# Kernel tuning notes

Measured on AMD Instinct MI355X. Metric: run time of the kernel, lower is better.

## Reference

```python
import jax, jax.numpy as jnp
import numpy as np
from jax import lax

C, H, W = 256, 56, 56
KP, STRIDE = 9, 2
M_CH, D, T = 64, 128, 16
TOPK = 32
SIGMA, ALPHA, TAU, EPS = 3.0, 10.0, 10.0, 1e-6
B = 4
N = H * W
PAD = KP // 2


def _build_M_P(h, w, s):
    ys = np.arange(0, h, s)
    xs = np.arange(0, w, s)
    ny, nx = len(ys), len(xs)
    N_, K_ = h * w, ny * nx
    by, bx = np.meshgrid(np.arange(h, dtype=np.float32), np.arange(w, dtype=np.float32), indexing='ij')
    bx = bx.reshape(-1)
    by = by.reshape(-1)
    fx, fy = bx / float(s), by / float(s)
    x0 = np.floor(fx).astype(np.int64)
    y0 = np.floor(fy).astype(np.int64)
    x0c = np.clip(x0, 0, nx - 1)
    x1c = np.clip(x0 + 1, 0, nx - 1)
    y0c = np.clip(y0, 0, ny - 1)
    y1c = np.clip(y0 + 1, 0, ny - 1)
    wx = fx - x0
    wy = fy - y0
    Mm = np.zeros((N_, K_), dtype=np.float32)
    rows = np.arange(N_)
    Mm[rows, y0c * nx + x0c] += (1 - wx) * (1 - wy)
    Mm[rows, y0c * nx + x1c] += wx * (1 - wy)
    Mm[rows, y1c * nx + x0c] += (1 - wx) * wy
    Mm[rows, y1c * nx + x1c] += wx * wy
    rs = Mm.sum(1, keepdims=True)
    rs[rs == 0] = 1.0
    Mm = Mm / rs
    P = np.stack([bx, by], axis=-1).astype(np.float32)  # (N,2) (x,y)
    return Mm, P


def _forward(feature_map, A_bank, pw_w, pw_b, proj_w, proj_b, r, M, P):
    def make_grid(A):  # affine_grid, align_corners=False
        xs = (2.0 * jnp.arange(W, dtype=jnp.float32) + 1.0) / W - 1.0
        ys = (2.0 * jnp.arange(H, dtype=jnp.float32) + 1.0) / H - 1.0
        gy, gx = jnp.meshgrid(ys, xs, indexing='ij')
        base = jnp.stack([gx, gy, jnp.ones_like(gx)], axis=-1)  # (H,W,3)
        return base @ A.T  # (H,W,2) normalized (x,y)

    def grid_sample(grid):  # bilinear, border padding, align_corners=False
        ix = ((grid[..., 0] + 1.0) * W - 1.0) / 2.0
        iy = ((grid[..., 1] + 1.0) * H - 1.0) / 2.0
        x0 = jnp.floor(ix)
        y0 = jnp.floor(iy)
        wx = ix - x0
        wy = iy - y0
        x0c = jnp.clip(x0, 0, W - 1).astype(jnp.int32)
        x1c = jnp.clip(x0 + 1, 0, W - 1).astype(jnp.int32)
        y0c = jnp.clip(y0, 0, H - 1).astype(jnp.int32)
        y1c = jnp.clip(y0 + 1, 0, H - 1).astype(jnp.int32)
        fm = feature_map.reshape(B, C, H * W)
        def g(yc, xc):
            return fm[:, :, (yc * W + xc).reshape(-1)].reshape(B, C, H, W)
        return (g(y0c, x0c) * (1 - wx) * (1 - wy) + g(y0c, x1c) * wx * (1 - wy)
                + g(y1c, x0c) * (1 - wx) * wy + g(y1c, x1c) * wx * wy)

    grids = jax.vmap(make_grid)(A_bank)          # (T,H,W,2)
    warped = jax.vmap(grid_sample)(grids)        # (T,B,C,H,W)

    # unfold(k,pad,stride) -> 1x1 conv -> spatial mean  ==  zero-padded avg-pool then linear
    pm = lax.reduce_window(warped, 0.0, lax.add,
                           (1, 1, 1, KP, KP), (1, 1, 1, STRIDE, STRIDE),
                           [(0, 0), (0, 0), (0, 0), (PAD, PAD), (PAD, PAD)]) / (KP * KP)
    Tn, Bn, Cn, Kh, Kw = pm.shape
    K = Kh * Kw
    pm = pm.reshape(Tn, Bn, Cn, K).transpose(0, 1, 3, 2)  # (T,B,K,C)
    x = pm @ pw_w.T + pw_b                                 # (T,B,K,m)
    z = x @ proj_w.T + proj_b                              # (T,B,K,d)
    z = z / jnp.maximum(jnp.linalg.norm(z, axis=-1, keepdims=True), EPS)
    Z = z.transpose(1, 0, 2, 3)                            # (B,T,K,d)

    s = jnp.einsum('btkd,d->btk', Z, r)
    wgt = jax.nn.softmax(TAU * s, axis=1)[..., None]
    g_emb = jnp.sum(wgt * Z, axis=1)                       # (B,K,d)

    E = jnp.einsum('nk,bkd->bnd', M, g_emb)
    E = E / jnp.maximum(jnp.linalg.norm(E, axis=-1, keepdims=True), EPS)

    d2 = jnp.sum((P[:, None, :] - P[None, :, :]) ** 2, axis=-1)  # (N,N)
    G = 1.0 - jnp.exp(-d2 / (2.0 * SIGMA ** 2))
    Saff = jnp.einsum('bnd,bmd->bnm', E, E) * G

    vals, idx = lax.top_k(Saff, TOPK)
    bidx = jnp.arange(B)[:, None, None]
    nidx = jnp.arange(N)[None, :, None]
    S_sp = jnp.zeros_like(Saff).at[bidx, nidx, idx].set(vals)
    A0 = jax.nn.softmax(ALPHA * S_sp, axis=-1) * jax.nn.softmax(ALPHA * S_sp, axis=-2)
    return E, A0


def setup_inputs() -> dict:
    key = jax.random.key(0)
    ks = jax.random.split(key, 6)
    feature_map = jax.random.normal(ks[0], (B, C, H, W), jnp.float32)
    ident = jnp.broadcast_to(jnp.array([[1.0, 0.0, 0.0], [0.0, 1.0, 0.0]], jnp.float32), (T, 2, 3))
    A_bank = ident + 0.1 * jax.random.normal(ks[1], (T, 2, 3), jnp.float32)
    pw_w = jax.random.normal(ks[2], (M_CH, C), jnp.float32) / np.sqrt(C).astype(np.float32)
    pw_b = jnp.zeros((M_CH,), jnp.float32)
    proj_w = jax.random.normal(ks[3], (D, M_CH), jnp.float32) / np.sqrt(M_CH).astype(np.float32)
    proj_b = jnp.zeros((D,), jnp.float32)
    r = 0.01 * jax.random.normal(ks[4], (D,), jnp.float32)
    Mnp, Pnp = _build_M_P(H, W, STRIDE)
    return {'feature_map': feature_map, 'A_bank': A_bank, 'pw_w': pw_w, 'pw_b': pw_b,
            'proj_w': proj_w, 'proj_b': proj_b, 'r': r,
            'M': jnp.asarray(Mnp), 'P': jnp.asarray(Pnp)}


def reference(feature_map, A_bank, pw_w, pw_b, proj_w, proj_b, r, M, P):
    return _forward(feature_map, A_bank, pw_w, pw_b, proj_w, proj_b, r, M, P)
```

## Files before the change

kernel.cpp:

```cpp
#include <hip/hip_runtime.h>
#include <hip/hip_bf16.h>
#include <hip/hip_fp16.h>

#define Hh 56
#define Ww 56
#define Cc 256
#define Tt 16
#define Bb 4
#define Nn 3136
#define Kk 784
#define KX 28
#define Dd 128
#define Mc 64
#define NTOP 32

__global__ __launch_bounds__(128) void k_wc(
    const float* __restrict__ pw_w, const float* __restrict__ pw_b,
    const float* __restrict__ proj_w, const float* __restrict__ proj_b,
    float* __restrict__ wct, float* __restrict__ bc) {
  int c = blockIdx.x;
  int d = threadIdx.x;
  float acc = 0.f;
  for (int m = 0; m < Mc; ++m) acc += proj_w[d * Mc + m] * pw_w[m * Cc + c];
  wct[c * Dd + d] = acc;
  if (c == 0) {
    float bb = proj_b[d];
    for (int m = 0; m < Mc; ++m) bb += proj_w[d * Mc + m] * pw_b[m];
    bc[d] = bb;
  }
}

__global__ __launch_bounds__(256) void k_mix(
    const float* __restrict__ fm, const float* __restrict__ wct, float* __restrict__ y) {
  int blk = blockIdx.x;
  int b = blk / 112;
  int n0 = (blk % 112) * 28;
  int tid = threadIdx.x;
  int d = tid & 127;
  int ng = tid >> 7;
  __shared__ float fm_s[64 * 28];
  __shared__ float wc_s[64 * Dd];
  float acc[14];
#pragma unroll
  for (int j = 0; j < 14; ++j) acc[j] = 0.f;
  const float* fb = fm + (size_t)b * Cc * Nn;
  for (int c0 = 0; c0 < Cc; c0 += 64) {
    for (int i = tid; i < 64 * 28; i += 256) {
      int c = i / 28, kx = i - c * 28;
      fm_s[i] = fb[(size_t)(c0 + c) * Nn + n0 + kx];
    }
    for (int i = tid; i < 64 * Dd; i += 256) wc_s[i] = wct[c0 * Dd + i];
    __syncthreads();
    for (int c = 0; c < 64; ++c) {
      float w = wc_s[c * Dd + d];
#pragma unroll
      for (int j = 0; j < 14; ++j) acc[j] += fm_s[c * 28 + ng * 14 + j] * w;
    }
    __syncthreads();
  }
  float* yo = y + ((size_t)b * Dd + d) * Nn + n0 + ng * 14;
#pragma unroll
  for (int j = 0; j < 14; ++j) yo[j] = acc[j];
}

__global__ __launch_bounds__(256) void k_fused_pool(
    const float* __restrict__ y, const float* __restrict__ Abank,
    const float* __restrict__ bc, float* __restrict__ zt) {
  int idx = blockIdx.x;
  int b = idx & 3;
  int dg = (idx >> 2) & 31;
  int t = idx >> 7;
  __shared__ float wsm[3136];
  __shared__ float rowp[1568];
  int tid = threadIdx.x;
  const float* A = Abank + t * 6;
  float a00 = A[0], a01 = A[1], a02 = A[2], a10 = A[3], a11 = A[4], a12 = A[5];
  int off[13];
  float wxa[13], wya[13];
#pragma unroll
  for (int j = 0; j < 13; ++j) {
    int e = tid + 256 * j;
    if (e < 3136) {
      int h = e / 56, w = e - h * 56;
      float gx = (2.0f * w + 1.0f) / 56.0f - 1.0f;
      float gy = (2.0f * h + 1.0f) / 56.0f - 1.0f;
      float u = a00 * gx + a01 * gy + a02;
      float v = a10 * gx + a11 * gy + a12;
      float ix = ((u + 1.0f) * 56.0f - 1.0f) * 0.5f;
      float iy = ((v + 1.0f) * 56.0f - 1.0f) * 0.5f;
      float x0f = floorf(ix), y0f = floorf(iy);
      wxa[j] = ix - x0f;
      wya[j] = iy - y0f;
      int x0 = (int)x0f, y0 = (int)y0f;
      int x0c = min(max(x0, 0), 55), x1c = min(max(x0 + 1, 0), 55);
      int y0c = min(max(y0, 0), 55), y1c = min(max(y0 + 1, 0), 55);
      off[j] = (y0c * 56 + x0c) | ((x1c - x0c) << 12) | ((y1c - y0c) << 13);
    }
  }
  for (int dd = 0; dd < 4; ++dd) {
    int d = dg * 4 + dd;
    const float* fc = y + ((size_t)b * Dd + d) * Nn;
    float bias = bc[d];
#pragma unroll
    for (int j = 0; j < 13; ++j) {
      int e = tid + 256 * j;
      if (e < 3136) {
        int pk = off[j];
        int base = pk & 4095;
        int dx = (pk >> 12) & 1;
        int dyy = (pk & (1 << 13)) ? 56 : 0;
        float v00 = fc[base], v01 = fc[base + dx];
        float v10 = fc[base + dyy], v11 = fc[base + dyy + dx];
        float wx = wxa[j], wy = wya[j];
        float top = v00 + wx * (v01 - v00);
        float bot = v10 + wx * (v11 - v10);
        wsm[e] = top + wy * (bot - top);
      }
    }
    __syncthreads();
    for (int e = tid; e < 1568; e += 256) {
      int h = e / 28, kx = e - h * 28;
      int xs = 2 * kx - 4;
      int lo = max(xs, 0), hi = min(xs + 8, 55);
      float s = 0.f;
      const float* wr = wsm + h * 56;
      for (int x = lo; x <= hi; ++x) s += wr[x];
      rowp[e] = s;
    }
    __syncthreads();
    float* zo = zt + ((size_t)(t * Bb + b) * Dd + d) * Kk;
    for (int e = tid; e < 784; e += 256) {
      int ky = e / 28, kx = e - ky * 28;
      int ys = 2 * ky - 4;
      int lo = max(ys, 0), hi = min(ys + 8, 55);
      float s = 0.f;
      for (int h = lo; h <= hi; ++h) s += rowp[h * 28 + kx];
      zo[e] = s * (1.0f / 81.0f) + bias;
    }
    __syncthreads();
  }
}

__global__ __launch_bounds__(256) void k_znorm(
    const float* __restrict__ zt, const float* __restrict__ r,
    float* __restrict__ z, float* __restrict__ s_arr) {
  int tb = blockIdx.x / 14;
  int k0 = (blockIdx.x % 14) * 56;
  int tid = threadIdx.x;
  __shared__ float ls[56 * 129];
  const float* zb = zt + (size_t)tb * Dd * Kk + k0;
  for (int i = tid; i < Dd * 56; i += 256) {
    int d = i / 56, kk = i - d * 56;
    ls[kk * 129 + d] = zb[(size_t)d * Kk + kk];
  }
  int lane = tid & 63;
  int wv = tid >> 6;
  float r0 = r[lane], r1 = r[lane + 64];
  __syncthreads();
  for (int p = 0; p < 14; ++p) {
    int k = p * 4 + wv;
    float z0 = ls[k * 129 + lane];
    float z1 = ls[k * 129 + 64 + lane];
    float ss = z0 * z0 + z1 * z1;
    for (int off = 32; off; off >>= 1) ss += __shfl_xor(ss, off);
    float inv = 1.0f / fmaxf(sqrtf(ss), 1e-6f);
    z0 *= inv; z1 *= inv;
    float* zr = z + ((size_t)tb * Kk + k0 + k) * Dd;
    zr[lane] = z0;
    zr[lane + 64] = z1;
    float sd = z0 * r0 + z1 * r1;
    for (int off = 32; off; off >>= 1) sd += __shfl_xor(sd, off);
    if (lane == 0) s_arr[(size_t)tb * Kk + k0 + k] = sd;
  }
}

__global__ __launch_bounds__(128) void k_gemb(
    const float* __restrict__ z, const float* __restrict__ s_arr, float* __restrict__ g) {
  int blk = blockIdx.x;
  int b = blk / Kk, k = blk % Kk;
  int d = threadIdx.x;
  float sv[Tt];
  float mx = -3.4e38f;
#pragma unroll
  for (int t = 0; t < Tt; ++t) {
    sv[t] = s_arr[(t * Bb + b) * Kk + k];
    mx = fmaxf(mx, sv[t]);
  }
  float sum = 0.f;
#pragma unroll
  for (int t = 0; t < Tt; ++t) {
    sv[t] = expf(10.0f * (sv[t] - mx));
    sum += sv[t];
  }
  float isum = 1.0f / sum;
  float acc = 0.f;
#pragma unroll
  for (int t = 0; t < Tt; ++t)
    acc += sv[t] * isum * z[((size_t)(t * Bb + b) * Kk + k) * Dd + d];
  g[((size_t)b * Kk + k) * Dd + d] = acc;
}

__global__ __launch_bounds__(64) void k_E(
    const float* __restrict__ Mmat, const float* __restrict__ g, float* __restrict__ E) {
  int row = blockIdx.x;
  int b = row / Nn, n = row % Nn;
  int y = n / Ww, x = n % Ww;
  int x0 = x >> 1, y0 = y >> 1;
  int x1 = min(x0 + 1, 27), y1 = min(y0 + 1, 27);
  bool hx = (x1 != x0), hy = (y1 != y0);
  int k00 = y0 * 28 + x0, k01 = y0 * 28 + x1, k10 = y1 * 28 + x0, k11 = y1 * 28 + x1;
  const float* Mr = Mmat + (size_t)n * Kk;
  float m00 = Mr[k00];
  float m01 = hx ? Mr[k01] : 0.f;
  float m10 = hy ? Mr[k10] : 0.f;
  float m11 = (hx && hy) ? Mr[k11] : 0.f;
  const float* gb = g + (size_t)b * Kk * Dd;
  int lane = threadIdx.x;
  int l2 = lane + 64;
  float a0 = m00 * gb[k00 * Dd + lane] + m01 * gb[k01 * Dd + lane] +
             m10 * gb[k10 * Dd + lane] + m11 * gb[k11 * Dd + lane];
  float a1 = m00 * gb[k00 * Dd + l2] + m01 * gb[k01 * Dd + l2] +
             m10 * gb[k10 * Dd + l2] + m11 * gb[k11 * Dd + l2];
  float ss = a0 * a0 + a1 * a1;
  for (int off = 32; off; off >>= 1) ss += __shfl_xor(ss, off);
  float inv = 1.0f / fmaxf(sqrtf(ss), 1e-6f);
  E[(size_t)row * Dd + lane] = a0 * inv;
  E[(size_t)row * Dd + l2] = a1 * inv;
}

__global__ __launch_bounds__(256) void k_saff(
    const float* __restrict__ E, const float* __restrict__ P, __half* __restrict__ S) {
  int blk = blockIdx.x;
  int b = blk / 1225;
  int rem = blk % 1225;
  int ti0 = (int)((sqrtf(8.f * rem + 1.f) - 1.f) * 0.5f);
  while ((ti0 + 1) * (ti0 + 2) / 2 <= rem) ++ti0;
  while (ti0 * (ti0 + 1) / 2 > rem) --ti0;
  int tj0 = rem - ti0 * (ti0 + 1) / 2;
  int i0 = ti0 * 64, j0 = tj0 * 64;
  __shared__ __align__(16) float Ei_s[64 * 68];
  __shared__ __align__(16) float Ej_s[64 * 68];
  __shared__ float s_pxi[64], s_pyi[64], s_pxj[64], s_pyj[64];
  int tid = threadIdx.x;
  const float* Eb = E + (size_t)b * Nn * Dd;
  if (tid < 64) {
    s_pxi[tid] = P[(i0 + tid) * 2];
    s_pyi[tid] = P[(i0 + tid) * 2 + 1];
    s_pxj[tid] = P[(j0 + tid) * 2];
    s_pyj[tid] = P[(j0 + tid) * 2 + 1];
  }
  int ti = tid >> 4, tj = tid & 15;
  int ib = ti * 4, jb = tj * 4;
  float acc[4][4];
#pragma unroll
  for (int a = 0; a < 4; ++a)
#pragma unroll
    for (int c = 0; c < 4; ++c) acc[a][c] = 0.f;
  for (int kc = 0; kc < Dd; kc += 64) {
    __syncthreads();
    for (int idx = tid; idx < 64 * 64; idx += 256) {
      int ii = idx >> 6, dd = idx & 63;
      Ei_s[dd * 68 + ii] = Eb[(size_t)(i0 + ii) * Dd + kc + dd];
      Ej_s[dd * 68 + ii] = Eb[(size_t)(j0 + ii) * Dd + kc + dd];
    }
    __syncthreads();
#pragma unroll 8
    for (int kk = 0; kk < 64; ++kk) {
      const float4 a = *reinterpret_cast<const float4*>(&Ei_s[kk * 68 + ib]);
      const float4 q = *reinterpret_cast<const float4*>(&Ej_s[kk * 68 + jb]);
      acc[0][0] += a.x * q.x; acc[0][1] += a.x * q.y; acc[0][2] += a.x * q.z; acc[0][3] += a.x * q.w;
      acc[1][0] += a.y * q.x; acc[1][1] += a.y * q.y; acc[1][2] += a.y * q.z; acc[1][3] += a.y * q.w;
      acc[2][0] += a.z * q.x; acc[2][1] += a.z * q.y; acc[2][2] += a.z * q.z; acc[2][3] += a.z * q.w;
      acc[3][0] += a.w * q.x; acc[3][1] += a.w * q.y; acc[3][2] += a.w * q.z; acc[3][3] += a.w * q.w;
    }
  }
  float outv[4][4];
#pragma unroll
  for (int di = 0; di < 4; ++di) {
    float px = s_pxi[ib + di], py = s_pyi[ib + di];
#pragma unroll
    for (int dj = 0; dj < 4; ++dj) {
      float dx = px - s_pxj[jb + dj];
      float dy = py - s_pyj[jb + dj];
      float gg = 1.0f - __expf(-(dx * dx + dy * dy) * (1.0f / 18.0f));
      outv[di][dj] = acc[di][dj] * gg;
    }
  }
  size_t ob = (size_t)b * Nn * Nn;
#pragma unroll
  for (int di = 0; di < 4; ++di) {
    __half2 h01 = __floats2half2_rn(outv[di][0], outv[di][1]);
    __half2 h23 = __floats2half2_rn(outv[di][2], outv[di][3]);
    __half2* p = reinterpret_cast<__half2*>(&S[ob + (size_t)(i0 + ib + di) * Nn + j0 + jb]);
    p[0] = h01; p[1] = h23;
  }
  if (i0 != j0) {
#pragma unroll
    for (int dj = 0; dj < 4; ++dj) {
      __half2 h01 = __floats2half2_rn(outv[0][dj], outv[1][dj]);
      __half2 h23 = __floats2half2_rn(outv[2][dj], outv[3][dj]);
      __half2* p = reinterpret_cast<__half2*>(&S[ob + (size_t)(j0 + jb + dj) * Nn + i0 + ib]);
      p[0] = h01; p[1] = h23;
    }
  }
}

__global__ __launch_bounds__(256) void k_topk(
    const __half* __restrict__ S16, const float* __restrict__ E,
    const float* __restrict__ P, float* __restrict__ topv, int* __restrict__ topi,
    float* __restrict__ dr, float* __restrict__ dc) {
  int row = blockIdx.x;
  int b = row / Nn, irow = row % Nn;
  int tid = threadIdx.x;
  const unsigned* Sr = reinterpret_cast<const unsigned*>(S16 + (size_t)row * Nn);
  __shared__ unsigned hist[256 * 8];
  __shared__ unsigned scan_s[256];
  __shared__ unsigned bcast[2];
  __shared__ unsigned sel_eq, sel_slot;
  __shared__ int sel_idx[NTOP];
  __shared__ float drow_s;
  unsigned pk[7];
#pragma unroll
  for (int j = 0; j < 7; ++j) {
    int c2 = tid + 256 * j;
    unsigned u = (c2 < Nn / 2) ? Sr[c2] : 0u;
    unsigned h0 = u & 0xFFFFu, h1 = u >> 16;
    unsigned k0 = h0 ^ ((h0 & 0x8000u) ? 0xFFFFu : 0x8000u);
    unsigned k1 = h1 ^ ((h1 & 0x8000u) ? 0xFFFFu : 0x8000u);
    if (c2 >= Nn / 2) { k0 = 0u; k1 = 0u; }
    pk[j] = k0 | (k1 << 16);
  }
  if (tid == 0) { sel_eq = 0; sel_slot = 0; drow_s = 0.f; }
  unsigned prefix = 0;
  unsigned k = NTOP;
  for (int pass = 0; pass < 2; ++pass) {
    int shift = 8 - 8 * pass;
    unsigned pmask = pass ? 0xFF00u : 0u;
#pragma unroll
    for (int i = 0; i < 8; ++i) hist[tid * 8 + i] = 0;
    __syncthreads();
#pragma unroll
    for (int j = 0; j < 7; ++j) {
      unsigned k0 = pk[j] & 0xFFFFu, k1 = pk[j] >> 16;
      if ((k0 & pmask) == (prefix & pmask))
        atomicAdd(&hist[((k0 >> shift) & 255u) * 8 + (tid & 7)], 1u);
      if ((k1 & pmask) == (prefix & pmask))
        atomicAdd(&hist[((k1 >> shift) & 255u) * 8 + (tid & 7)], 1u);
    }
    __syncthreads();
    unsigned cnt = 0;
#pragma unroll
    for (int i = 0; i < 8; ++i) cnt += hist[tid * 8 + i];
    unsigned run = cnt;
    scan_s[tid] = run;
    for (int st = 1; st < 256; st <<= 1) {
      __syncthreads();
      unsigned add = (tid + st < 256) ? scan_s[tid + st] : 0u;
      __syncthreads();
      run += add;
      scan_s[tid] = run;
    }
    unsigned incl = run;
    unsigned excl = incl - cnt;
    if (excl < k && k <= incl) {
      bcast[0] = prefix | ((unsigned)tid << shift);
      bcast[1] = k - excl;
    }
    __syncthreads();
    prefix = bcast[0];
    k = bcast[1];
    __syncthreads();
  }
  unsigned T = prefix;
#pragma unroll
  for (int j = 0; j < 7; ++j) {
    int c2 = tid + 256 * j;
    if (c2 < Nn / 2) {
      unsigned k0 = pk[j] & 0xFFFFu, k1 = pk[j] >> 16;
      bool take0 = (k0 > T) || (k0 == T && atomicAdd(&sel_eq, 1u) < k);
      if (take0) { unsigned slot = atomicAdd(&sel_slot, 1u); sel_idx[slot] = 2 * c2; }
      bool take1 = (k1 > T) || (k1 == T && atomicAdd(&sel_eq, 1u) < k);
      if (take1) { unsigned slot = atomicAdd(&sel_slot, 1u); sel_idx[slot] = 2 * c2 + 1; }
    }
  }
  __syncthreads();
  int sel = tid >> 3, part = tid & 7;
  int col = sel_idx[sel];
  const float* Ei = E + ((size_t)b * Nn + irow) * Dd;
  const float* Ej = E + ((size_t)b * Nn + col) * Dd;
  float v = 0.f;
#pragma unroll
  for (int d0 = 0; d0 < 16; ++d0) {
    int d = part * 16 + d0;
    v += Ei[d] * Ej[d];
  }
  v += __shfl_xor(v, 1);
  v += __shfl_xor(v, 2);
  v += __shfl_xor(v, 4);
  if (part == 0) {
    float dx = P[irow * 2] - P[col * 2];
    float dy = P[irow * 2 + 1] - P[col * 2 + 1];
    float gg = 1.0f - __expf(-(dx * dx + dy * dy) * (1.0f / 18.0f));
    v *= gg;
    topv[(size_t)row * NTOP + sel] = v;
    topi[(size_t)row * NTOP + sel] = col;
    float e = __expf(10.f * v);
    atomicAdd(&dc[b * Nn + col], e - 1.f);
    atomicAdd(&drow_s, e);
  }
  __syncthreads();
  if (tid == 0) dr[row] = (float)(Nn - NTOP) + drow_s;
}

__global__ void k_dcinit(float* __restrict__ dc) {
  int i = blockIdx.x * 256 + threadIdx.x;
  if (i < Bb * Nn) dc[i] = (float)Nn;
}

__global__ void k_inv(float* __restrict__ dr, float* __restrict__ dc) {
  int i = blockIdx.x * 256 + threadIdx.x;
  if (i < Bb * Nn) {
    dr[i] = 1.0f / dr[i];
    dc[i] = 1.0f / dc[i];
  }
}

__global__ __launch_bounds__(256) void k_basefix(
    const float* __restrict__ invdr, const float* __restrict__ invdc,
    const float* __restrict__ topv, const int* __restrict__ topi,
    float* __restrict__ A0) {
  int row = blockIdx.x;
  int b = row / Nn;
  float idr = invdr[row];
  const float4* dc4 = reinterpret_cast<const float4*>(invdc + b * Nn);
  float4* out4 = reinterpret_cast<float4*>(A0 + (size_t)row * Nn);
  for (int j = threadIdx.x; j < Nn / 4; j += 256) {
    float4 c = dc4[j];
    float4 o = {idr * c.x, idr * c.y, idr * c.z, idr * c.w};
    out4[j] = o;
  }
  __syncthreads();
  if (threadIdx.x < NTOP) {
    int gidx = row * NTOP + threadIdx.x;
    int col = topi[gidx];
    float e = __expf(10.f * topv[gidx]);
    A0[(size_t)row * Nn + col] = e * e * idr * invdc[b * Nn + col];
  }
}

extern "C" void kernel_launch(void* const* d_in, const int* in_sizes, int n_in,
                              void* d_out, int out_size, void* d_ws, size_t ws_size,
                              hipStream_t stream) {
  const float* fm     = (const float*)d_in[0];
  const float* Abank  = (const float*)d_in[1];
  const float* pw_w   = (const float*)d_in[2];
  const float* pw_b   = (const float*)d_in[3];
  const float* proj_w = (const float*)d_in[4];
  const float* proj_b = (const float*)d_in[5];
  const float* r      = (const float*)d_in[6];
  const float* Mmat   = (const float*)d_in[7];
  const float* P      = (const float*)d_in[8];
  float* out = (float*)d_out;
  float* E  = out;
  float* A0 = out + (size_t)Bb * Nn * Dd;
  __half* S16 = (__half*)A0;

  float* ws = (float*)d_ws;
  float* y     = ws;
  float* zt    = ws + 1605632;
  float* z     = ws + 8028160;
  float* wct   = ws + 14450688;
  float* bcv   = ws + 14483456;
  float* s_arr = ws + 14483584;
  float* g     = ws + 14533760;
  float* topv  = ws + 14935168;
  int*   topi  = (int*)(ws + 15336576);
  float* dr    = ws + 15737984;
  float* dc    = ws + 15750528;

  hipLaunchKernelGGL(k_wc, dim3(Cc), dim3(128), 0, stream, pw_w, pw_b, proj_w, proj_b, wct, bcv);
  hipLaunchKernelGGL(k_mix, dim3(448), dim3(256), 0, stream, fm, wct, y);
  hipLaunchKernelGGL(k_fused_pool, dim3(2048), dim3(256), 0, stream, y, Abank, bcv, zt);
  hipLaunchKernelGGL(k_znorm, dim3(64 * 14), dim3(256), 0, stream, zt, r, z, s_arr);
  hipLaunchKernelGGL(k_gemb, dim3(Bb * Kk), dim3(128), 0, stream, z, s_arr, g);
  hipLaunchKernelGGL(k_E, dim3(Bb * Nn), dim3(64), 0, stream, Mmat, g, E);
  hipLaunchKernelGGL(k_saff, dim3(Bb * 1225), dim3(256), 0, stream, E, P, S16);
  hipLaunchKernelGGL(k_dcinit, dim3(49), dim3(256), 0, stream, dc);
  hipLaunchKernelGGL(k_topk, dim3(Bb * Nn), dim3(256), 0, stream, S16, E, P, topv, topi, dr, dc);
  hipLaunchKernelGGL(k_inv, dim3(49), dim3(256), 0, stream, dr, dc);
  hipLaunchKernelGGL(k_basefix, dim3(Bb * Nn), dim3(256), 0, stream, dr, dc, topv, topi, A0);
}
```

Measured before the change: 515.8 us.

## Compute spatial affinity with fp16 MFMA instead of fp32 shared-memory FMA

k_E now also writes an fp16 copy of the normalized embeddings, and k_saff computes each 64x64 tile with MFMA 16x16x32 f16 instructions that load operands directly from global memory. The shared-memory staging is removed, and pixel coordinates are derived from the index instead of being read from P. This targets the FMA-bound fp32 tile GEMM but lowers input precision to fp16. Output stores become scalar half writes with a strided mirrored write, which may hurt store coalescing.

```diff
diff --git a/kernel.cpp b/kernel.cpp
--- a/kernel.cpp
+++ b/kernel.cpp
@@ -13,6 +13,9 @@
 #define Dd 128
 #define Mc 64
 #define NTOP 32
+
+typedef __attribute__((ext_vector_type(8))) _Float16 f16x8;
+typedef __attribute__((ext_vector_type(4))) float f32x4;
 
 __global__ __launch_bounds__(128) void k_wc(
     const float* __restrict__ pw_w, const float* __restrict__ pw_b,
@@ -201,7 +204,8 @@
 }
 
 __global__ __launch_bounds__(64) void k_E(
-    const float* __restrict__ Mmat, const float* __restrict__ g, float* __restrict__ E) {
+    const float* __restrict__ Mmat, const float* __restrict__ g,
+    float* __restrict__ E, _Float16* __restrict__ E16) {
   int row = blockIdx.x;
   int b = row / Nn, n = row % Nn;
   int y = n / Ww, x = n % Ww;
@@ -224,12 +228,15 @@
   float ss = a0 * a0 + a1 * a1;
   for (int off = 32; off; off >>= 1) ss += __shfl_xor(ss, off);
   float inv = 1.0f / fmaxf(sqrtf(ss), 1e-6f);
-  E[(size_t)row * Dd + lane] = a0 * inv;
-  E[(size_t)row * Dd + l2] = a1 * inv;
+  float e0 = a0 * inv, e1 = a1 * inv;
+  E[(size_t)row * Dd + lane] = e0;
+  E[(size_t)row * Dd + l2] = e1;
+  E16[(size_t)row * Dd + lane] = (_Float16)e0;
+  E16[(size_t)row * Dd + l2] = (_Float16)e1;
 }
 
 __global__ __launch_bounds__(256) void k_saff(
-    const float* __restrict__ E, const float* __restrict__ P, __half* __restrict__ S) {
+    const _Float16* __restrict__ E16, __half* __restrict__ S) {
   int blk = blockIdx.x;
   int b = blk / 1225;
   int rem = blk % 1225;
@@ -238,69 +245,59 @@
   while (ti0 * (ti0 + 1) / 2 > rem) --ti0;
   int tj0 = rem - ti0 * (ti0 + 1) / 2;
   int i0 = ti0 * 64, j0 = tj0 * 64;
-  __shared__ __align__(16) float Ei_s[64 * 68];
-  __shared__ __align__(16) float Ej_s[64 * 68];
-  __shared__ float s_pxi[64], s_pyi[64], s_pxj[64], s_pyj[64];
-  int tid = threadIdx.x;
-  const float* Eb = E + (size_t)b * Nn * Dd;
-  if (tid < 64) {
-    s_pxi[tid] = P[(i0 + tid) * 2];
-    s_pyi[tid] = P[(i0 + tid) * 2 + 1];
-    s_pxj[tid] = P[(j0 + tid) * 2];
-    s_pyj[tid] = P[(j0 + tid) * 2 + 1];
-  }
-  int ti = tid >> 4, tj = tid & 15;
-  int ib = ti * 4, jb = tj * 4;
-  float acc[4][4];
-#pragma unroll
-  for (int a = 0; a < 4; ++a)
-#pragma unroll
-    for (int c = 0; c < 4; ++c) acc[a][c] = 0.f;
-  for (int kc = 0; kc < Dd; kc += 64) {
-    __syncthreads();
-    for (int idx = tid; idx < 64 * 64; idx += 256) {
-      int ii = idx >> 6, dd = idx & 63;
-      Ei_s[dd * 68 + ii] = Eb[(size_t)(i0 + ii) * Dd + kc + dd];
-      Ej_s[dd * 68 + ii] = Eb[(size_t)(j0 + ii) * Dd + kc + dd];
-    }
-    __syncthreads();
-#pragma unroll 8
-    for (int kk = 0; kk < 64; ++kk) {
-      const float4 a = *reinterpret_cast<const float4*>(&Ei_s[kk * 68 + ib]);
-      const float4 q = *reinterpret_cast<const float4*>(&Ej_s[kk * 68 + jb]);
-      acc[0][0] += a.x * q.x; acc[0][1] += a.x * q.y; acc[0][2] += a.x * q.z; acc[0][3] += a.x * q.w;
-      acc[1][0] += a.y * q.x; acc[1][1] += a.y * q.y; acc[1][2] += a.y * q.z; acc[1][3] += a.y * q.w;
-      acc[2][0] += a.z * q.x; acc[2][1] += a.z * q.y; acc[2][2] += a.z * q.z; acc[2][3] += a.z * q.w;
-      acc[3][0] += a.w * q.x; acc[3][1] += a.w * q.y; acc[3][2] += a.w * q.z; acc[3][3] += a.w * q.w;
-    }
-  }
-  float outv[4][4];
-#pragma unroll
-  for (int di = 0; di < 4; ++di) {
-    float px = s_pxi[ib + di], py = s_pyi[ib + di];
-#pragma unroll
-    for (int dj = 0; dj < 4; ++dj) {
-      float dx = px - s_pxj[jb + dj];
-      float dy = py - s_pyj[jb + dj];
-      float gg = 1.0f - __expf(-(dx * dx + dy * dy) * (1.0f / 18.0f));
-      outv[di][dj] = acc[di][dj] * gg;
-    }
+  int wave = threadIdx.x >> 6, lane = threadIdx.x & 63;
+  int wr = wave >> 1, wc = wave & 1;
+  int lr = lane & 15, lk = lane >> 4;
+  int ibase = i0 + wr * 32;
+  int jbase = j0 + wc * 32;
+  const _Float16* Eb = E16 + (size_t)b * Nn * Dd;
+  f32x4 acc00 = {0.f, 0.f, 0.f, 0.f};
+  f32x4 acc01 = acc00, acc10 = acc00, acc11 = acc00;
+#pragma unroll
+  for (int ks = 0; ks < 4; ++ks) {
+    int ko = ks * 32 + lk * 8;
+    f16x8 a0 = *reinterpret_cast<const f16x8*>(Eb + (size_t)(ibase + lr) * Dd + ko);
+    f16x8 a1 = *reinterpret_cast<const f16x8*>(Eb + (size_t)(ibase + 16 + lr) * Dd + ko);
+    f16x8 b0 = *reinterpret_cast<const f16x8*>(Eb + (size_t)(jbase + lr) * Dd + ko);
+    f16x8 b1 = *reinterpret_cast<const f16x8*>(Eb + (size_t)(jbase + 16 + lr) * Dd + ko);
+    acc00 = __builtin_amdgcn_mfma_f32_16x16x32_f16(a0, b0, acc00, 0, 0, 0);
+    acc01 = __builtin_amdgcn_mfma_f32_16x16x32_f16(a0, b1, acc01, 0, 0, 0);
+    acc10 = __builtin_amdgcn_mfma_f32_16x16x32_f16(a1, b0, acc10, 0, 0, 0);
+    acc11 = __builtin_amdgcn_mfma_f32_16x16x32_f16(a1, b1, acc11, 0, 0, 0);
   }
   size_t ob = (size_t)b * Nn * Nn;
-#pragma unroll
-  for (int di = 0; di < 4; ++di) {
-    __half2 h01 = __floats2half2_rn(outv[di][0], outv[di][1]);
-    __half2 h23 = __floats2half2_rn(outv[di][2], outv[di][3]);
-    __half2* p = reinterpret_cast<__half2*>(&S[ob + (size_t)(i0 + ib + di) * Nn + j0 + jb]);
-    p[0] = h01; p[1] = h23;
-  }
-  if (i0 != j0) {
-#pragma unroll
-    for (int dj = 0; dj < 4; ++dj) {
-      __half2 h01 = __floats2half2_rn(outv[0][dj], outv[1][dj]);
-      __half2 h23 = __floats2half2_rn(outv[2][dj], outv[3][dj]);
-      __half2* p = reinterpret_cast<__half2*>(&S[ob + (size_t)(j0 + jb + dj) * Nn + i0 + ib]);
-      p[0] = h01; p[1] = h23;
+  int gj[2];
+  float xj[2], yj[2];
+#pragma unroll
+  for (int tj = 0; tj < 2; ++tj) {
+    gj[tj] = jbase + tj * 16 + lr;
+    int yv = gj[tj] / 56;
+    yj[tj] = (float)yv;
+    xj[tj] = (float)(gj[tj] - yv * 56);
+  }
+  bool mirror = (i0 != j0);
+#pragma unroll
+  for (int ti = 0; ti < 2; ++ti) {
+#pragma unroll
+    for (int q = 0; q < 4; ++q) {
+      int gi = ibase + ti * 16 + lk * 4 + q;
+      int yiv = gi / 56;
+      float yi = (float)yiv;
+      float xi = (float)(gi - yiv * 56);
+#pragma unroll
+      for (int tj = 0; tj < 2; ++tj) {
+        float a;
+        if (ti == 0 && tj == 0) a = acc00[q];
+        else if (ti == 0 && tj == 1) a = acc01[q];
+        else if (ti == 1 && tj == 0) a = acc10[q];
+        else a = acc11[q];
+        float dx = xi - xj[tj];
+        float dy = yi - yj[tj];
+        float gg = 1.0f - __expf(-(dx * dx + dy * dy) * (1.0f / 18.0f));
+        __half hv = __float2half(a * gg);
+        S[ob + (size_t)gi * Nn + gj[tj]] = hv;
+        if (mirror) S[ob + (size_t)gj[tj] * Nn + gi] = hv;
+      }
     }
   }
 }
@@ -477,14 +474,15 @@
   int*   topi  = (int*)(ws + 15336576);
   float* dr    = ws + 15737984;
   float* dc    = ws + 15750528;
+  _Float16* E16 = (_Float16*)(ws + 15763072);
 
   hipLaunchKernelGGL(k_wc, dim3(Cc), dim3(128), 0, stream, pw_w, pw_b, proj_w, proj_b, wct, bcv);
   hipLaunchKernelGGL(k_mix, dim3(448), dim3(256), 0, stream, fm, wct, y);
   hipLaunchKernelGGL(k_fused_pool, dim3(2048), dim3(256), 0, stream, y, Abank, bcv, zt);
   hipLaunchKernelGGL(k_znorm, dim3(64 * 14), dim3(256), 0, stream, zt, r, z, s_arr);
   hipLaunchKernelGGL(k_gemb, dim3(Bb * Kk), dim3(128), 0, stream, z, s_arr, g);
-  hipLaunchKernelGGL(k_E, dim3(Bb * Nn), dim3(64), 0, stream, Mmat, g, E);
-  hipLaunchKernelGGL(k_saff, dim3(Bb * 1225), dim3(256), 0, stream, E, P, S16);
+  hipLaunchKernelGGL(k_E, dim3(Bb * Nn), dim3(64), 0, stream, Mmat, g, E, E16);
+  hipLaunchKernelGGL(k_saff, dim3(Bb * 1225), dim3(256), 0, stream, E16, S16);
   hipLaunchKernelGGL(k_dcinit, dim3(49), dim3(256), 0, stream, dc);
   hipLaunchKernelGGL(k_topk, dim3(Bb * Nn), dim3(256), 0, stream, S16, E, P, topv, topi, dr, dc);
   hipLaunchKernelGGL(k_inv, dim3(49), dim3(256), 0, stream, dr, dc);
```

Measured after the change: 489.8 us. 1.05x faster.
